# Optimization experiments

Measured on AMD Instinct MI355X. Metric: run time of the kernel, lower is better.

The kernel has to match this reference:

```python
import jax, jax.numpy as jnp
import numpy as np

D_MODEL = 1024
N_HEADS = 16
HEAD_DIM = D_MODEL // N_HEADS


def setup_inputs() -> dict:
    key = jax.random.key(0)
    k1, k2, k3 = jax.random.split(key, 3)
    x = jax.random.normal(k1, (4, 2048, D_MODEL), dtype=jnp.float32)
    # nn.Linear(d_model, 3*d_model, bias=False): weight [3*d_model, d_model]
    w_qkv = jax.random.normal(k2, (3 * D_MODEL, D_MODEL), dtype=jnp.float32) / np.sqrt(D_MODEL)
    w_out = jax.random.normal(k3, (D_MODEL, D_MODEL), dtype=jnp.float32) / np.sqrt(D_MODEL)
    return {"x": x, "w_qkv": w_qkv, "w_out": w_out}


def reference(x, w_qkv, w_out):
    B, T, C = x.shape
    qkv = jnp.einsum('btc,fc->btf', x, w_qkv)  # [B,T,3C]
    q, k, v = jnp.split(qkv, 3, axis=-1)

    def heads(t):
        return t.reshape(B, T, N_HEADS, HEAD_DIM).transpose(0, 2, 1, 3)  # [B,H,T,D]

    q, k, v = heads(q), heads(k), heads(v)
    scale = 1.0 / np.sqrt(HEAD_DIM).astype(np.float32)
    attn = jnp.einsum('bhqd,bhkd->bhqk', q, k) * scale  # [B,H,T,T]
    causal = jnp.tril(jnp.ones((T, T), dtype=bool))
    attn = jnp.where(causal[None, None], attn, -jnp.inf)
    attn = jax.nn.softmax(attn, axis=-1)
    out = jnp.einsum('bhqk,bhkd->bhqd', attn, v)
    out = out.transpose(0, 2, 1, 3).reshape(B, T, C)
    return jnp.einsum('btc,fc->btf', out, w_out)
```

## Files before the change

### kernel.cpp

```cpp
#include <hip/hip_runtime.h>
#include <hip/hip_bf16.h>
#include <type_traits>


typedef __attribute__((ext_vector_type(8))) short bf16x8;
typedef __attribute__((ext_vector_type(4))) float f32x4;

#define LDS_AS(p) ((__attribute__((address_space(3))) void*)(p))
#define GLB_AS(p) ((const __attribute__((address_space(1))) void*)(p))

__global__ __launch_bounds__(256) void cvt_f32_bf16(const float* __restrict__ in,
                                                    __hip_bfloat16* __restrict__ out,
                                                    int n4) {
  int i = blockIdx.x * 256 + threadIdx.x;
  if (i >= n4) return;
  float4 v = reinterpret_cast<const float4*>(in)[i];
  __hip_bfloat16 b0 = __float2bfloat16(v.x);
  __hip_bfloat16 b1 = __float2bfloat16(v.y);
  __hip_bfloat16 b2 = __float2bfloat16(v.z);
  __hip_bfloat16 b3 = __float2bfloat16(v.w);
  ushort4 u;
  u.x = *reinterpret_cast<unsigned short*>(&b0);
  u.y = *reinterpret_cast<unsigned short*>(&b1);
  u.z = *reinterpret_cast<unsigned short*>(&b2);
  u.w = *reinterpret_cast<unsigned short*>(&b3);
  reinterpret_cast<ushort4*>(out)[i] = u;
}

template <typename TOUT>
__global__ __launch_bounds__(256) void gemm_bt(const __hip_bfloat16* __restrict__ A,
                                               const __hip_bfloat16* __restrict__ B,
                                               TOUT* __restrict__ C,
                                               int M, int N, int K) {
  __shared__ __hip_bfloat16 As[128 * 64];
  __shared__ __hip_bfloat16 Bs[128 * 64];
  const int tid = threadIdx.x;
  const int lane = tid & 63;
  const int wid = tid >> 6;
  const int l15 = lane & 15, l4 = lane >> 4;
  const int m0 = blockIdx.x * 128, n0 = blockIdx.y * 128;
  const int wr = (wid >> 1) * 64;
  const int wc = (wid & 1) * 64;
  f32x4 acc[4][4] = {};

  for (int kt = 0; kt < K; kt += 64) {
#pragma unroll
    for (int i = 0; i < 4; ++i) {
      const int slot = i * 256 + tid;
      const int row = slot >> 3, c8 = slot & 7;
      __builtin_amdgcn_global_load_lds(GLB_AS(A + (size_t)(m0 + row) * K + kt + c8 * 8),
                                       LDS_AS((char*)As + slot * 16), 16, 0, 0);
      __builtin_amdgcn_global_load_lds(GLB_AS(B + (size_t)(n0 + row) * K + kt + c8 * 8),
                                       LDS_AS((char*)Bs + slot * 16), 16, 0, 0);
    }
    __syncthreads();
#pragma unroll
    for (int kk = 0; kk < 2; ++kk) {
      bf16x8 af[4], bfr[4];
#pragma unroll
      for (int mi = 0; mi < 4; ++mi)
        af[mi] = *reinterpret_cast<const bf16x8*>(As + (wr + mi * 16 + l15) * 64 + kk * 32 + l4 * 8);
#pragma unroll
      for (int ni = 0; ni < 4; ++ni)
        bfr[ni] = *reinterpret_cast<const bf16x8*>(Bs + (wc + ni * 16 + l15) * 64 + kk * 32 + l4 * 8);
#pragma unroll
      for (int mi = 0; mi < 4; ++mi)
#pragma unroll
        for (int ni = 0; ni < 4; ++ni)
          acc[mi][ni] = __builtin_amdgcn_mfma_f32_16x16x32_bf16(af[mi], bfr[ni], acc[mi][ni], 0, 0, 0);
    }
    __syncthreads();
  }
#pragma unroll
  for (int mi = 0; mi < 4; ++mi)
#pragma unroll
    for (int ni = 0; ni < 4; ++ni)
#pragma unroll
      for (int j = 0; j < 4; ++j) {
        const int m = m0 + wr + mi * 16 + l4 * 4 + j;
        const int n = n0 + wc + ni * 16 + l15;
        if constexpr (std::is_same<TOUT, float>::value)
          C[(size_t)m * N + n] = acc[mi][ni][j];
        else
          C[(size_t)m * N + n] = __float2bfloat16(acc[mi][ni][j]);
      }
}

__global__ __launch_bounds__(512, 2) void attn_causal(const __hip_bfloat16* __restrict__ qkv,
                                                      __hip_bfloat16* __restrict__ o) {
  constexpr int T = 2048, F = 3072, C = 1024;
  __shared__ __hip_bfloat16 Ks[2][64 * 72];
  __shared__ __hip_bfloat16 Vts[2][64 * 72];
  __shared__ __hip_bfloat16 Ps[8][16 * 72];
  const int tid = threadIdx.x;
  const int wid = tid >> 6, lane = tid & 63;
  const int l15 = lane & 15, l4 = lane >> 4;
  const int x = blockIdx.x, h = blockIdx.y, b = blockIdx.z;
  const int qt = (wid < 4) ? x : (7 - x);
  const int nt = 4 * (7 - x) + 4;
  const int tmax = 4 * qt + (wid & 3);
  const int hoff = h * 64;
  const __hip_bfloat16* base = qkv + (size_t)b * T * F;
  const int Q0 = qt * 256 + (wid & 3) * 64;

  constexpr float SC = 0.125f * 1.44269504088896f;

  bf16x8 aq[4][2];
#pragma unroll
  for (int f = 0; f < 4; ++f)
#pragma unroll
    for (int kk = 0; kk < 2; ++kk) {
      bf16x8 q = *reinterpret_cast<const bf16x8*>(base + (size_t)(Q0 + f * 16 + l15) * F + hoff + kk * 32 + l4 * 8);
#pragma unroll
      for (int e = 0; e < 8; ++e) {
        const unsigned short raw = (unsigned short)q[e];
        const float fv = __uint_as_float((unsigned)raw << 16) * SC;
        __hip_bfloat16 qs = __float2bfloat16(fv);
        q[e] = *reinterpret_cast<short*>(&qs);
      }
      aq[f][kk] = q;
    }

  f32x4 acc[4][4] = {};
  float mrun[4], lrun[4];
#pragma unroll
  for (int f = 0; f < 4; ++f) { mrun[f] = -1e30f; lrun[f] = 0.f; }

  const int sV = tid;
  const int sK = tid - 256;
  bf16x8 sreg0, sreg1;
  if (wid < 4) {
    const size_t vr = (size_t)(2 * (sV >> 3)) * F + hoff + 2 * C + (sV & 7) * 8;
    sreg0 = *reinterpret_cast<const bf16x8*>(base + vr);
    sreg1 = *reinterpret_cast<const bf16x8*>(base + vr + F);
  } else {
    sreg0 = *reinterpret_cast<const bf16x8*>(base + (size_t)(sK >> 3) * F + hoff + C + (sK & 7) * 8);
    sreg1 = *reinterpret_cast<const bf16x8*>(base + (size_t)(32 + (sK >> 3)) * F + hoff + C + (sK & 7) * 8);
  }

  for (int t = 0; t < nt; ++t) {
    const int cur = t & 1;
    if (wid < 4) {
      const unsigned short* a0 = reinterpret_cast<const unsigned short*>(&sreg0);
      const unsigned short* a1 = reinterpret_cast<const unsigned short*>(&sreg1);
      const int c8 = sV & 7, r2 = sV >> 3;
      unsigned pk[8], tw[8], pkr[8];
#pragma unroll
      for (int j = 0; j < 8; ++j) pk[j] = (unsigned)a0[j] | ((unsigned)a1[j] << 16);
#pragma unroll
      for (int j = 0; j < 8; ++j) tw[j] = (c8 & 4) ? pk[(j + 4) & 7] : pk[j];
#pragma unroll
      for (int j = 0; j < 8; ++j) pkr[j] = (c8 & 2) ? tw[(j + 2) & 7] : tw[j];
#pragma unroll
      for (int j = 0; j < 8; ++j) tw[j] = (c8 & 1) ? pkr[(j + 1) & 7] : pkr[j];
#pragma unroll
      for (int jj = 0; jj < 8; ++jj) {
        const int d = c8 * 8 + ((jj + c8) & 7);
        *reinterpret_cast<unsigned*>(&Vts[cur][d * 72 + 2 * r2]) = tw[jj];
      }
    } else {
      *reinterpret_cast<bf16x8*>(&Ks[cur][(sK >> 3) * 72 + (sK & 7) * 8]) = sreg0;
      *reinterpret_cast<bf16x8*>(&Ks[cur][(32 + (sK >> 3)) * 72 + (sK & 7) * 8]) = sreg1;
    }
    __syncthreads();
    if (t + 1 < nt) {
      const int kn = (t + 1) * 64;
      if (wid < 4) {
        const size_t vr = (size_t)(kn + 2 * (sV >> 3)) * F + hoff + 2 * C + (sV & 7) * 8;
        sreg0 = *reinterpret_cast<const bf16x8*>(base + vr);
        sreg1 = *reinterpret_cast<const bf16x8*>(base + vr + F);
      } else {
        sreg0 = *reinterpret_cast<const bf16x8*>(base + (size_t)(kn + (sK >> 3)) * F + hoff + C + (sK & 7) * 8);
        sreg1 = *reinterpret_cast<const bf16x8*>(base + (size_t)(kn + 32 + (sK >> 3)) * F + hoff + C + (sK & 7) * 8);
      }
    }
    if (t > tmax) continue;
    const bool diag = (t == tmax);

    bf16x8 kf[4][2], vf[4][2];
#pragma unroll
    for (int kt = 0; kt < 4; ++kt)
#pragma unroll
      for (int kk = 0; kk < 2; ++kk)
        kf[kt][kk] = *reinterpret_cast<const bf16x8*>(&Ks[cur][(kt * 16 + l15) * 72 + kk * 32 + l4 * 8]);
#pragma unroll
    for (int di = 0; di < 4; ++di)
#pragma unroll
      for (int kk = 0; kk < 2; ++kk)
        vf[di][kk] = *reinterpret_cast<const bf16x8*>(&Vts[cur][(di * 16 + l15) * 72 + kk * 32 + l4 * 8]);

    __hip_bfloat16* pw = Ps[wid];
#pragma unroll
    for (int f = 0; f < 4; ++f) {
      f32x4 s[4];
#pragma unroll
      for (int kt = 0; kt < 4; ++kt) {
        f32x4 z = {};
        z = __builtin_amdgcn_mfma_f32_16x16x32_bf16(kf[kt][0], aq[f][0], z, 0, 0, 0);
        z = __builtin_amdgcn_mfma_f32_16x16x32_bf16(kf[kt][1], aq[f][1], z, 0, 0, 0);
        s[kt] = z;
      }
      if (diag) {
        const int ql = f * 16 + l15;
#pragma unroll
        for (int kt = 0; kt < 4; ++kt)
#pragma unroll
          for (int j = 0; j < 4; ++j) {
            const int kvl = kt * 16 + l4 * 4 + j;
            s[kt][j] = (kvl <= ql) ? s[kt][j] : -1e30f;
          }
      }

      float t0 = fmaxf(fmaxf(s[0][0], s[0][1]), s[0][2]);
      float t1 = fmaxf(fmaxf(s[0][3], s[1][0]), s[1][1]);
      float t2 = fmaxf(fmaxf(s[1][2], s[1][3]), s[2][0]);
      float t3 = fmaxf(fmaxf(s[2][1], s[2][2]), s[2][3]);
      float t4 = fmaxf(fmaxf(s[3][0], s[3][1]), s[3][2]);
      float mt = fmaxf(fmaxf(fmaxf(t0, t1), fmaxf(t2, t3)), fmaxf(t4, s[3][3]));
      mt = fmaxf(mt, __shfl_xor(mt, 16, 64));
      mt = fmaxf(mt, __shfl_xor(mt, 32, 64));
      const bool defer = __all(mt <= mrun[f] + 8.f);
      const float mnew = defer ? mrun[f] : fmaxf(mrun[f], mt);
      float rs = 0.f;
#pragma unroll
      for (int kt = 0; kt < 4; ++kt) {
        float p0 = exp2f(s[kt][0] - mnew), p1 = exp2f(s[kt][1] - mnew);
        float p2 = exp2f(s[kt][2] - mnew), p3 = exp2f(s[kt][3] - mnew);
        s[kt][0] = p0; s[kt][1] = p1; s[kt][2] = p2; s[kt][3] = p3;
        rs += (p0 + p1) + (p2 + p3);
      }
      rs += __shfl_xor(rs, 16, 64);
      rs += __shfl_xor(rs, 32, 64);
      if (defer) {
        lrun[f] += rs;
      } else {
        const float sco = exp2f(mrun[f] - mnew);
        lrun[f] = lrun[f] * sco + rs;
        mrun[f] = mnew;
#pragma unroll
        for (int di = 0; di < 4; ++di) acc[f][di] *= sco;
      }

#pragma unroll
      for (int kt = 0; kt < 4; ++kt) {
        unsigned w0, w1;
        asm("v_cvt_pk_bf16_f32 %0, %1, %2" : "=v"(w0) : "v"(s[kt][0]), "v"(s[kt][1]));
        asm("v_cvt_pk_bf16_f32 %0, %1, %2" : "=v"(w1) : "v"(s[kt][2]), "v"(s[kt][3]));
        unsigned long long dw = (unsigned long long)w0 | ((unsigned long long)w1 << 32);
        *reinterpret_cast<unsigned long long*>(&pw[l15 * 72 + kt * 16 + l4 * 4]) = dw;
      }
      asm volatile("s_waitcnt lgkmcnt(0)" ::: "memory");
      bf16x8 pa0 = *reinterpret_cast<const bf16x8*>(pw + l15 * 72 + l4 * 8);
      bf16x8 pa1 = *reinterpret_cast<const bf16x8*>(pw + l15 * 72 + 32 + l4 * 8);

#pragma unroll
      for (int di = 0; di < 4; ++di) {
        acc[f][di] = __builtin_amdgcn_mfma_f32_16x16x32_bf16(vf[di][0], pa0, acc[f][di], 0, 0, 0);
        acc[f][di] = __builtin_amdgcn_mfma_f32_16x16x32_bf16(vf[di][1], pa1, acc[f][di], 0, 0, 0);
      }
    }
  }

#pragma unroll
  for (int f = 0; f < 4; ++f) {
    const float inv = 1.0f / lrun[f];
    __hip_bfloat16* op = o + (size_t)((size_t)b * T + Q0 + f * 16 + l15) * C + hoff;
#pragma unroll
    for (int di = 0; di < 4; ++di) {
      ushort4 u;
      __hip_bfloat16 e0 = __float2bfloat16(acc[f][di][0] * inv);
      __hip_bfloat16 e1 = __float2bfloat16(acc[f][di][1] * inv);
      __hip_bfloat16 e2 = __float2bfloat16(acc[f][di][2] * inv);
      __hip_bfloat16 e3 = __float2bfloat16(acc[f][di][3] * inv);
      u.x = *reinterpret_cast<unsigned short*>(&e0);
      u.y = *reinterpret_cast<unsigned short*>(&e1);
      u.z = *reinterpret_cast<unsigned short*>(&e2);
      u.w = *reinterpret_cast<unsigned short*>(&e3);
      *reinterpret_cast<ushort4*>(op + di * 16 + l4 * 4) = u;
    }
  }
}

extern "C" void kernel_launch(void* const* d_in, const int* in_sizes, int n_in,
                              void* d_out, int out_size, void* d_ws, size_t ws_size,
                              hipStream_t stream) {
  const float* x = (const float*)d_in[0];
  const float* w_qkv = (const float*)d_in[1];
  const float* w_out = (const float*)d_in[2];
  float* out = (float*)d_out;

  constexpr int B = 4, T = 2048, C = 1024, F = 3 * C;
  constexpr int M = B * T;

  __hip_bfloat16* xb = (__hip_bfloat16*)d_ws;
  __hip_bfloat16* wqkvb = xb + (size_t)M * C;
  __hip_bfloat16* woutb = wqkvb + (size_t)F * C;
  __hip_bfloat16* qkvb = woutb + (size_t)C * C;
  __hip_bfloat16* attnb = qkvb + (size_t)M * F;

  cvt_f32_bf16<<<(M * C / 4 + 255) / 256, 256, 0, stream>>>(x, xb, M * C / 4);
  cvt_f32_bf16<<<(F * C / 4 + 255) / 256, 256, 0, stream>>>(w_qkv, wqkvb, F * C / 4);
  cvt_f32_bf16<<<(C * C / 4 + 255) / 256, 256, 0, stream>>>(w_out, woutb, C * C / 4);

  gemm_bt<__hip_bfloat16><<<dim3(M / 128, F / 128), 256, 0, stream>>>(xb, wqkvb, qkvb, M, F, C);

  attn_causal<<<dim3(4, 16, B), 512, 0, stream>>>(qkvb, attnb);

  gemm_bt<float><<<dim3(M / 128, C / 128), 256, 0, stream>>>(attnb, woutb, out, M, C, C);
}
```

Before: 231.1 us.

## Batch attention S/PV MFMAs across row groups and fuse conversion launches

The attention inner loop is restructured to compute all four 16-row score tiles first, then run softmax for all of them, then write all P tiles to LDS with a single wait, and finally issue all PV MFMAs back to back. s_setprio is raised around the MFMA bursts, and the P staging buffer grows to one tile per row group. Occupancy hint drops to one block per SIMD because the extra live registers would not fit two. The three fp32-to-bf16 conversion launches are merged into one kernel to save launch overhead.

After: 240.2 us. 1.04x slower.

```diff
diff --git a/kernel.cpp b/kernel.cpp
--- a/kernel.cpp
+++ b/kernel.cpp
@@ -9,11 +9,19 @@
 #define LDS_AS(p) ((__attribute__((address_space(3))) void*)(p))
 #define GLB_AS(p) ((const __attribute__((address_space(1))) void*)(p))
 
-__global__ __launch_bounds__(256) void cvt_f32_bf16(const float* __restrict__ in,
-                                                    __hip_bfloat16* __restrict__ out,
-                                                    int n4) {
+__global__ __launch_bounds__(256) void cvt3_f32_bf16(const float* __restrict__ a,
+                                                     const float* __restrict__ b,
+                                                     const float* __restrict__ c,
+                                                     __hip_bfloat16* __restrict__ oa,
+                                                     __hip_bfloat16* __restrict__ ob,
+                                                     __hip_bfloat16* __restrict__ oc,
+                                                     int na4, int nb4, int nc4) {
   int i = blockIdx.x * 256 + threadIdx.x;
-  if (i >= n4) return;
+  const float* in; __hip_bfloat16* out;
+  if (i < na4) { in = a; out = oa; }
+  else if (i < na4 + nb4) { in = b; out = ob; i -= na4; }
+  else if (i < na4 + nb4 + nc4) { in = c; out = oc; i -= na4 + nb4; }
+  else return;
   float4 v = reinterpret_cast<const float4*>(in)[i];
   __hip_bfloat16 b0 = __float2bfloat16(v.x);
   __hip_bfloat16 b1 = __float2bfloat16(v.y);
@@ -86,12 +94,12 @@
       }
 }
 
-__global__ __launch_bounds__(512, 2) void attn_causal(const __hip_bfloat16* __restrict__ qkv,
+__global__ __launch_bounds__(512, 1) void attn_causal(const __hip_bfloat16* __restrict__ qkv,
                                                       __hip_bfloat16* __restrict__ o) {
   constexpr int T = 2048, F = 3072, C = 1024;
   __shared__ __hip_bfloat16 Ks[2][64 * 72];
   __shared__ __hip_bfloat16 Vts[2][64 * 72];
-  __shared__ __hip_bfloat16 Ps[8][16 * 72];
+  __shared__ __hip_bfloat16 Ps[8][4][16 * 72];
   const int tid = threadIdx.x;
   const int wid = tid >> 6, lane = tid & 63;
   const int l15 = lane & 15, l4 = lane >> 4;
@@ -189,17 +197,21 @@
       for (int kk = 0; kk < 2; ++kk)
         vf[di][kk] = *reinterpret_cast<const bf16x8*>(&Vts[cur][(di * 16 + l15) * 72 + kk * 32 + l4 * 8]);
 
-    __hip_bfloat16* pw = Ps[wid];
-#pragma unroll
-    for (int f = 0; f < 4; ++f) {
-      f32x4 s[4];
+    f32x4 s[4][4];
+    __builtin_amdgcn_s_setprio(1);
+#pragma unroll
+    for (int f = 0; f < 4; ++f)
 #pragma unroll
       for (int kt = 0; kt < 4; ++kt) {
         f32x4 z = {};
         z = __builtin_amdgcn_mfma_f32_16x16x32_bf16(kf[kt][0], aq[f][0], z, 0, 0, 0);
         z = __builtin_amdgcn_mfma_f32_16x16x32_bf16(kf[kt][1], aq[f][1], z, 0, 0, 0);
-        s[kt] = z;
-      }
+        s[f][kt] = z;
+      }
+    __builtin_amdgcn_s_setprio(0);
+
+#pragma unroll
+    for (int f = 0; f < 4; ++f) {
       if (diag) {
         const int ql = f * 16 + l15;
 #pragma unroll
@@ -207,16 +219,15 @@
 #pragma unroll
           for (int j = 0; j < 4; ++j) {
             const int kvl = kt * 16 + l4 * 4 + j;
-            s[kt][j] = (kvl <= ql) ? s[kt][j] : -1e30f;
+            s[f][kt][j] = (kvl <= ql) ? s[f][kt][j] : -1e30f;
           }
       }
-
-      float t0 = fmaxf(fmaxf(s[0][0], s[0][1]), s[0][2]);
-      float t1 = fmaxf(fmaxf(s[0][3], s[1][0]), s[1][1]);
-      float t2 = fmaxf(fmaxf(s[1][2], s[1][3]), s[2][0]);
-      float t3 = fmaxf(fmaxf(s[2][1], s[2][2]), s[2][3]);
-      float t4 = fmaxf(fmaxf(s[3][0], s[3][1]), s[3][2]);
-      float mt = fmaxf(fmaxf(fmaxf(t0, t1), fmaxf(t2, t3)), fmaxf(t4, s[3][3]));
+      float t0 = fmaxf(fmaxf(s[f][0][0], s[f][0][1]), s[f][0][2]);
+      float t1 = fmaxf(fmaxf(s[f][0][3], s[f][1][0]), s[f][1][1]);
+      float t2 = fmaxf(fmaxf(s[f][1][2], s[f][1][3]), s[f][2][0]);
+      float t3 = fmaxf(fmaxf(s[f][2][1], s[f][2][2]), s[f][2][3]);
+      float t4 = fmaxf(fmaxf(s[f][3][0], s[f][3][1]), s[f][3][2]);
+      float mt = fmaxf(fmaxf(fmaxf(t0, t1), fmaxf(t2, t3)), fmaxf(t4, s[f][3][3]));
       mt = fmaxf(mt, __shfl_xor(mt, 16, 64));
       mt = fmaxf(mt, __shfl_xor(mt, 32, 64));
       const bool defer = __all(mt <= mrun[f] + 8.f);
@@ -224,9 +235,9 @@
       float rs = 0.f;
 #pragma unroll
       for (int kt = 0; kt < 4; ++kt) {
-        float p0 = exp2f(s[kt][0] - mnew), p1 = exp2f(s[kt][1] - mnew);
-        float p2 = exp2f(s[kt][2] - mnew), p3 = exp2f(s[kt][3] - mnew);
-        s[kt][0] = p0; s[kt][1] = p1; s[kt][2] = p2; s[kt][3] = p3;
+        float p0 = exp2f(s[f][kt][0] - mnew), p1 = exp2f(s[f][kt][1] - mnew);
+        float p2 = exp2f(s[f][kt][2] - mnew), p3 = exp2f(s[f][kt][3] - mnew);
+        s[f][kt][0] = p0; s[f][kt][1] = p1; s[f][kt][2] = p2; s[f][kt][3] = p3;
         rs += (p0 + p1) + (p2 + p3);
       }
       rs += __shfl_xor(rs, 16, 64);
@@ -240,25 +251,38 @@
 #pragma unroll
         for (int di = 0; di < 4; ++di) acc[f][di] *= sco;
       }
-
+    }
+
+#pragma unroll
+    for (int f = 0; f < 4; ++f) {
+      __hip_bfloat16* pw = &Ps[wid][f][0];
 #pragma unroll
       for (int kt = 0; kt < 4; ++kt) {
         unsigned w0, w1;
-        asm("v_cvt_pk_bf16_f32 %0, %1, %2" : "=v"(w0) : "v"(s[kt][0]), "v"(s[kt][1]));
-        asm("v_cvt_pk_bf16_f32 %0, %1, %2" : "=v"(w1) : "v"(s[kt][2]), "v"(s[kt][3]));
+        asm("v_cvt_pk_bf16_f32 %0, %1, %2" : "=v"(w0) : "v"(s[f][kt][0]), "v"(s[f][kt][1]));
+        asm("v_cvt_pk_bf16_f32 %0, %1, %2" : "=v"(w1) : "v"(s[f][kt][2]), "v"(s[f][kt][3]));
         unsigned long long dw = (unsigned long long)w0 | ((unsigned long long)w1 << 32);
         *reinterpret_cast<unsigned long long*>(&pw[l15 * 72 + kt * 16 + l4 * 4]) = dw;
       }
-      asm volatile("s_waitcnt lgkmcnt(0)" ::: "memory");
-      bf16x8 pa0 = *reinterpret_cast<const bf16x8*>(pw + l15 * 72 + l4 * 8);
-      bf16x8 pa1 = *reinterpret_cast<const bf16x8*>(pw + l15 * 72 + 32 + l4 * 8);
-
+    }
+    asm volatile("s_waitcnt lgkmcnt(0)" ::: "memory");
+
+    bf16x8 pa[4][2];
+#pragma unroll
+    for (int f = 0; f < 4; ++f) {
+      const __hip_bfloat16* pw = &Ps[wid][f][0];
+      pa[f][0] = *reinterpret_cast<const bf16x8*>(pw + l15 * 72 + l4 * 8);
+      pa[f][1] = *reinterpret_cast<const bf16x8*>(pw + l15 * 72 + 32 + l4 * 8);
+    }
+    __builtin_amdgcn_s_setprio(1);
+#pragma unroll
+    for (int f = 0; f < 4; ++f)
 #pragma unroll
       for (int di = 0; di < 4; ++di) {
-        acc[f][di] = __builtin_amdgcn_mfma_f32_16x16x32_bf16(vf[di][0], pa0, acc[f][di], 0, 0, 0);
-        acc[f][di] = __builtin_amdgcn_mfma_f32_16x16x32_bf16(vf[di][1], pa1, acc[f][di], 0, 0, 0);
-      }
-    }
+        acc[f][di] = __builtin_amdgcn_mfma_f32_16x16x32_bf16(vf[di][0], pa[f][0], acc[f][di], 0, 0, 0);
+        acc[f][di] = __builtin_amdgcn_mfma_f32_16x16x32_bf16(vf[di][1], pa[f][1], acc[f][di], 0, 0, 0);
+      }
+    __builtin_amdgcn_s_setprio(0);
   }
 
 #pragma unroll
@@ -298,9 +322,9 @@
   __hip_bfloat16* qkvb = woutb + (size_t)C * C;
   __hip_bfloat16* attnb = qkvb + (size_t)M * F;
 
-  cvt_f32_bf16<<<(M * C / 4 + 255) / 256, 256, 0, stream>>>(x, xb, M * C / 4);
-  cvt_f32_bf16<<<(F * C / 4 + 255) / 256, 256, 0, stream>>>(w_qkv, wqkvb, F * C / 4);
-  cvt_f32_bf16<<<(C * C / 4 + 255) / 256, 256, 0, stream>>>(w_out, woutb, C * C / 4);
+  constexpr int na4 = M * C / 4, nb4 = F * C / 4, nc4 = C * C / 4;
+  cvt3_f32_bf16<<<(na4 + nb4 + nc4 + 255) / 256, 256, 0, stream>>>(
+      x, w_qkv, w_out, xb, wqkvb, woutb, na4, nb4, nc4);
 
   gemm_bt<__hip_bfloat16><<<dim3(M / 128, F / 128), 256, 0, stream>>>(xb, wqkvb, qkvb, M, F, C);
 
```

## Double-buffer GEMM LDS tiles and fuse three convert launches into one

Applied to the files above, without the earlier changes.

The bf16 GEMM now keeps two LDS buffers per operand. It issues the global_load_lds prefetch for the next K-tile before running the MFMAs on the current tile, so the kernel needs one barrier per iteration instead of two. This is meant to hide global load latency behind the matrix math. The cost is double the LDS footprint (64KB per block), which may lower occupancy. The three separate f32-to-bf16 conversion launches are also merged into a single kernel that branches on the flat index, saving launch overhead and tail effects.

Result: no change. 227.2 us (-1.7%).

```diff
diff --git a/kernel.cpp b/kernel.cpp
--- a/kernel.cpp
+++ b/kernel.cpp
@@ -9,11 +9,19 @@
 #define LDS_AS(p) ((__attribute__((address_space(3))) void*)(p))
 #define GLB_AS(p) ((const __attribute__((address_space(1))) void*)(p))
 
-__global__ __launch_bounds__(256) void cvt_f32_bf16(const float* __restrict__ in,
-                                                    __hip_bfloat16* __restrict__ out,
-                                                    int n4) {
+__global__ __launch_bounds__(256) void cvt3_f32_bf16(const float* __restrict__ a,
+                                                     const float* __restrict__ b,
+                                                     const float* __restrict__ c,
+                                                     __hip_bfloat16* __restrict__ oa,
+                                                     __hip_bfloat16* __restrict__ ob,
+                                                     __hip_bfloat16* __restrict__ oc,
+                                                     int na4, int nb4, int nc4) {
   int i = blockIdx.x * 256 + threadIdx.x;
-  if (i >= n4) return;
+  const float* in; __hip_bfloat16* out;
+  if (i < na4) { in = a; out = oa; }
+  else if (i < na4 + nb4) { in = b; out = ob; i -= na4; }
+  else if (i < na4 + nb4 + nc4) { in = c; out = oc; i -= na4 + nb4; }
+  else return;
   float4 v = reinterpret_cast<const float4*>(in)[i];
   __hip_bfloat16 b0 = __float2bfloat16(v.x);
   __hip_bfloat16 b1 = __float2bfloat16(v.y);
@@ -32,8 +40,8 @@
                                                const __hip_bfloat16* __restrict__ B,
                                                TOUT* __restrict__ C,
                                                int M, int N, int K) {
-  __shared__ __hip_bfloat16 As[128 * 64];
-  __shared__ __hip_bfloat16 Bs[128 * 64];
+  __shared__ __hip_bfloat16 As[2][128 * 64];
+  __shared__ __hip_bfloat16 Bs[2][128 * 64];
   const int tid = threadIdx.x;
   const int lane = tid & 63;
   const int wid = tid >> 6;
@@ -41,35 +49,51 @@
   const int m0 = blockIdx.x * 128, n0 = blockIdx.y * 128;
   const int wr = (wid >> 1) * 64;
   const int wc = (wid & 1) * 64;
+  const int NT = K >> 6;
   f32x4 acc[4][4] = {};
 
-  for (int kt = 0; kt < K; kt += 64) {
-#pragma unroll
-    for (int i = 0; i < 4; ++i) {
-      const int slot = i * 256 + tid;
-      const int row = slot >> 3, c8 = slot & 7;
-      __builtin_amdgcn_global_load_lds(GLB_AS(A + (size_t)(m0 + row) * K + kt + c8 * 8),
-                                       LDS_AS((char*)As + slot * 16), 16, 0, 0);
-      __builtin_amdgcn_global_load_lds(GLB_AS(B + (size_t)(n0 + row) * K + kt + c8 * 8),
-                                       LDS_AS((char*)Bs + slot * 16), 16, 0, 0);
-    }
-    __syncthreads();
+#pragma unroll
+  for (int i = 0; i < 4; ++i) {
+    const int slot = i * 256 + tid;
+    const int row = slot >> 3, c8 = slot & 7;
+    __builtin_amdgcn_global_load_lds(GLB_AS(A + (size_t)(m0 + row) * K + c8 * 8),
+                                     LDS_AS((char*)As[0] + slot * 16), 16, 0, 0);
+    __builtin_amdgcn_global_load_lds(GLB_AS(B + (size_t)(n0 + row) * K + c8 * 8),
+                                     LDS_AS((char*)Bs[0] + slot * 16), 16, 0, 0);
+  }
+  __syncthreads();
+
+  int cur = 0;
+  for (int t = 0; t < NT; ++t) {
+    if (t + 1 < NT) {
+      const int kt = (t + 1) << 6;
+#pragma unroll
+      for (int i = 0; i < 4; ++i) {
+        const int slot = i * 256 + tid;
+        const int row = slot >> 3, c8 = slot & 7;
+        __builtin_amdgcn_global_load_lds(GLB_AS(A + (size_t)(m0 + row) * K + kt + c8 * 8),
+                                         LDS_AS((char*)As[cur ^ 1] + slot * 16), 16, 0, 0);
+        __builtin_amdgcn_global_load_lds(GLB_AS(B + (size_t)(n0 + row) * K + kt + c8 * 8),
+                                         LDS_AS((char*)Bs[cur ^ 1] + slot * 16), 16, 0, 0);
+      }
+    }
 #pragma unroll
     for (int kk = 0; kk < 2; ++kk) {
       bf16x8 af[4], bfr[4];
 #pragma unroll
       for (int mi = 0; mi < 4; ++mi)
-        af[mi] = *reinterpret_cast<const bf16x8*>(As + (wr + mi * 16 + l15) * 64 + kk * 32 + l4 * 8);
+        af[mi] = *reinterpret_cast<const bf16x8*>(&As[cur][(wr + mi * 16 + l15) * 64 + kk * 32 + l4 * 8]);
 #pragma unroll
       for (int ni = 0; ni < 4; ++ni)
-        bfr[ni] = *reinterpret_cast<const bf16x8*>(Bs + (wc + ni * 16 + l15) * 64 + kk * 32 + l4 * 8);
+        bfr[ni] = *reinterpret_cast<const bf16x8*>(&Bs[cur][(wc + ni * 16 + l15) * 64 + kk * 32 + l4 * 8]);
 #pragma unroll
       for (int mi = 0; mi < 4; ++mi)
 #pragma unroll
         for (int ni = 0; ni < 4; ++ni)
           acc[mi][ni] = __builtin_amdgcn_mfma_f32_16x16x32_bf16(af[mi], bfr[ni], acc[mi][ni], 0, 0, 0);
     }
-    __syncthreads();
+    if (t + 1 < NT) __syncthreads();
+    cur ^= 1;
   }
 #pragma unroll
   for (int mi = 0; mi < 4; ++mi)
@@ -298,9 +322,9 @@
   __hip_bfloat16* qkvb = woutb + (size_t)C * C;
   __hip_bfloat16* attnb = qkvb + (size_t)M * F;
 
-  cvt_f32_bf16<<<(M * C / 4 + 255) / 256, 256, 0, stream>>>(x, xb, M * C / 4);
-  cvt_f32_bf16<<<(F * C / 4 + 255) / 256, 256, 0, stream>>>(w_qkv, wqkvb, F * C / 4);
-  cvt_f32_bf16<<<(C * C / 4 + 255) / 256, 256, 0, stream>>>(w_out, woutb, C * C / 4);
+  constexpr int na4 = M * C / 4, nb4 = F * C / 4, nc4 = C * C / 4;
+  cvt3_f32_bf16<<<(na4 + nb4 + nc4 + 255) / 256, 256, 0, stream>>>(
+      x, w_qkv, w_out, xb, wqkvb, woutb, na4, nb4, nc4);
 
   gemm_bt<__hip_bfloat16><<<dim3(M / 128, F / 128), 256, 0, stream>>>(xb, wqkvb, qkvb, M, F, C);
 
```
